# Optimization experiments

Hardware: AMD Instinct MI355X
Metric: run time of the kernel (lower is better)

## Reference

```python
import jax, jax.numpy as jnp
import numpy as np

B, N_GENES, N_SETS, G = 256, 10000, 1000, 128   # batch, input_dim, output_dim, geneset_size
H1, H2 = 64, 32                                  # hidden_dims
EPS = 1e-5                                       # BatchNorm1d eps


def _batchnorm(h, gamma, beta):
    # BatchNorm1d in training mode: biased batch stats over the batch axis
    mean = jnp.mean(h, axis=0, keepdims=True)
    var = jnp.mean(jnp.square(h - mean), axis=0, keepdims=True)
    return (h - mean) * jax.lax.rsqrt(var + EPS) * gamma + beta


def setup_inputs() -> dict:
    key = jax.random.key(0)
    ks = jax.random.split(key, 7)
    # Adjacency with exactly G distinct ones per column -> gather index list [N_SETS, G]
    rng = np.random.default_rng(0)
    gene_idx = np.argsort(rng.random((N_SETS, N_GENES)), axis=1)[:, :G]
    gene_idx = jnp.asarray(np.sort(gene_idx, axis=1), dtype=jnp.int32)

    x = jax.random.normal(ks[0], (B, N_GENES), jnp.float32)
    s1, s2, s3 = 1.0 / np.sqrt(G), 1.0 / np.sqrt(H1), 1.0 / np.sqrt(H2)
    W1 = jax.random.uniform(ks[1], (N_SETS, G, H1), jnp.float32, -s1, s1)
    b1 = jax.random.uniform(ks[2], (N_SETS, H1), jnp.float32, -s1, s1)
    W2 = jax.random.uniform(ks[3], (N_SETS, H1, H2), jnp.float32, -s2, s2)
    b2 = jax.random.uniform(ks[4], (N_SETS, H2), jnp.float32, -s2, s2)
    W3 = jax.random.uniform(ks[5], (N_SETS, H2), jnp.float32, -s3, s3)
    b3 = jax.random.uniform(ks[6], (N_SETS,), jnp.float32, -s3, s3)
    g1 = jnp.ones((N_SETS, H1), jnp.float32)
    be1 = jnp.zeros((N_SETS, H1), jnp.float32)
    g2 = jnp.ones((N_SETS, H2), jnp.float32)
    be2 = jnp.zeros((N_SETS, H2), jnp.float32)
    return {"x": x, "gene_idx": gene_idx, "W1": W1, "b1": b1, "g1": g1, "be1": be1,
            "W2": W2, "b2": b2, "g2": g2, "be2": be2, "W3": W3, "b3": b3}


def reference(x, gene_idx, W1, b1, g1, be1, W2, b2, g2, be2, W3, b3):
    # Per-geneset gather: x[:, adj[:,i]==1] for all i at once -> [B, S, G]
    xg = x[:, gene_idx]
    # Linear -> ReLU -> BatchNorm (per geneset, grouped GEMM)
    h = jax.nn.relu(jnp.einsum('bsg,sgh->bsh', xg, W1) + b1)
    h = _batchnorm(h, g1, be1)
    h = jax.nn.relu(jnp.einsum('bsh,shk->bsk', h, W2) + b2)
    h = _batchnorm(h, g2, be2)
    # Final Linear(H2 -> 1) -> ReLU, concatenated over genesets -> [B, S]
    out = jax.nn.relu(jnp.einsum('bsh,sh->bs', h, W3) + b3)
    return out
```

## Files before the change

kernel.cpp:

```cpp
#include <hip/hip_runtime.h>
#include <stdint.h>

#define BB 256
#define NG 10000
#define NS 1000
#define GG 128
#define H1 64
#define H2 32
#define EPSV 1e-5f


typedef unsigned short ushortT;
typedef __attribute__((ext_vector_type(4))) short short4v;
typedef __attribute__((ext_vector_type(8))) short short8v;
typedef __attribute__((ext_vector_type(4))) float float4v;

__device__ __forceinline__ float bf2f(ushortT u) {
    union { uint32_t i; float f; } v; v.i = ((uint32_t)u) << 16; return v.f;
}
__device__ __forceinline__ ushortT f2bf(float f) {
    union { float f; uint32_t i; } v; v.f = f;
    uint32_t x = v.i;
    return (ushortT)((x + 0x7fffu + ((x >> 16) & 1u)) >> 16);
}
__device__ __forceinline__ uint32_t pack2(ushortT lo, ushortT hi) {
    return (uint32_t)lo | ((uint32_t)hi << 16);
}
__device__ __forceinline__ bool probe_f32(const void* g1) {
    return ((*(const uint32_t*)g1) & 0xFFFFu) == 0u;
}
__device__ __forceinline__ float loadf(const void* p, int i, bool isf) {
    return isf ? ((const float*)p)[i] : bf2f(((const ushortT*)p)[i]);
}
__device__ __forceinline__ ushortT loadbf(const void* p, size_t i, bool isf) {
    return isf ? f2bf(((const float*)p)[i]) : ((const ushortT*)p)[i];
}

__global__ __launch_bounds__(256) void k_transpose(const void* __restrict__ x,
                                                   ushortT* __restrict__ xT,
                                                   const void* __restrict__ g1p) {
    __shared__ ushortT tile[64][66];
    const bool isf = probe_f32(g1p);
    const int tx = threadIdx.x & 63;
    const int tz = threadIdx.x >> 6;
    const int j0 = blockIdx.x * 64;
    const int b0 = blockIdx.y * 64;
    const int j = j0 + tx;
#pragma unroll
    for (int k = 0; k < 16; ++k) {
        int bl = tz * 16 + k;
        ushortT v = 0;
        if (j < NG) v = loadbf(x, (size_t)(b0 + bl) * NG + j, isf);
        tile[bl][tx] = v;
    }
    __syncthreads();
#pragma unroll
    for (int k = 0; k < 16; ++k) {
        int jl = tz * 16 + k;
        int jw = j0 + jl;
        if (jw < NG) xT[jw * BB + b0 + tx] = tile[tx][jl];
    }
}

__global__ __launch_bounds__(256, 4) void k_main(
    const ushortT* __restrict__ xT, const int* __restrict__ gidx,
    const void* __restrict__ W1, const void* __restrict__ W2,
    const void* __restrict__ b1, const void* __restrict__ g1, const void* __restrict__ be1,
    const void* __restrict__ b2, const void* __restrict__ g2, const void* __restrict__ be2,
    const void* __restrict__ W3, const void* __restrict__ b3,
    void* __restrict__ out) {
    __shared__ ushortT xg[BB * 68];
    __shared__ ushortT w1s[64 * 36];

    char* xgc = (char*)xg;
    float* redf = (float*)w1s;
    ushortT* w2s = w1s;

    const bool isf = probe_f32(g1);
    const int s = blockIdx.x;
    const int t = threadIdx.x;
    const int w = t >> 6;
    const int lane = t & 63;
    const int l16 = lane & 15;
    const int quad = lane >> 4;
    const size_t base1 = (size_t)s * (GG * H1);
    const size_t base2 = (size_t)s * (H1 * H2);

#define HOLEI(i)   (*(int*)(xgc + ((i) >> 1) * 136 + 128 + ((i) & 1) * 4))
#define HOLEF(r0, k) (*(float*)(xgc + ((r0) + ((k) >> 1)) * 136 + 128 + ((k) & 1) * 4))

    float b1v[4], w3v[2], b2v[2];
#pragma unroll
    for (int nt = 0; nt < 4; ++nt) b1v[nt] = loadf(b1, s * H1 + nt * 16 + l16, isf);
#pragma unroll
    for (int nt = 0; nt < 2; ++nt) {
        b2v[nt] = loadf(b2, s * H2 + nt * 16 + l16, isf);
        w3v[nt] = loadf(W3, s * H2 + nt * 16 + l16, isf);
    }
    const float b3v = loadf(b3, s, isf);
    float g1v = 0.f, be1v = 0.f, g2v = 0.f, be2v = 0.f;
    if (t < 64) { g1v = loadf(g1, s * H1 + t, isf); be1v = loadf(be1, s * H1 + t, isf); }
    if (t < 32) { g2v = loadf(g2, s * H2 + t, isf); be2v = loadf(be2, s * H2 + t, isf); }

    ushortT w2r[8];
    {
        const int k2 = t & 31, h0 = (t >> 5) * 8;
#pragma unroll
        for (int j = 0; j < 8; ++j) w2r[j] = loadbf(W2, base2 + (size_t)(h0 + j) * H2 + k2, isf);
    }

    if (t < GG) HOLEI(t) = gidx[s * GG + t];

    auto stageW1 = [&](int q) {
#pragma unroll
        for (int rep = 0; rep < 2; ++rep) {
            const int el = rep * 256 + t;
            const int e4 = q * 512 + el;
            const int g = el >> 4;
            const int h0 = (el & 15) * 4;
            ushortT u0, u1, u2, u3;
            if (isf) {
                float4 v = *(const float4*)((const float*)W1 + base1 + (size_t)e4 * 4);
                u0 = f2bf(v.x); u1 = f2bf(v.y); u2 = f2bf(v.z); u3 = f2bf(v.w);
            } else {
                uint2 v = *(const uint2*)((const ushortT*)W1 + base1 + (size_t)e4 * 4);
                u0 = (ushortT)v.x; u1 = (ushortT)(v.x >> 16);
                u2 = (ushortT)v.y; u3 = (ushortT)(v.y >> 16);
            }
            w1s[(h0 + 0) * 36 + g] = u0;
            w1s[(h0 + 1) * 36 + g] = u1;
            w1s[(h0 + 2) * 36 + g] = u2;
            w1s[(h0 + 3) * 36 + g] = u3;
        }
    };
    stageW1(0);
    __syncthreads();

    float4v acc1[4][4];
#pragma unroll
    for (int mt = 0; mt < 4; ++mt)
#pragma unroll
        for (int nt = 0; nt < 4; ++nt) acc1[mt][nt] = (float4v){0.f, 0.f, 0.f, 0.f};

#pragma unroll
    for (int c = 0; c < 2; ++c) {
#pragma unroll
        for (int gq = 0; gq < 8; ++gq) {
            const int i0 = c * 64 + gq * 8;
            int2 p0 = *(const int2*)(xgc + (i0 >> 1) * 136 + 128);
            int2 p1 = *(const int2*)(xgc + ((i0 >> 1) + 1) * 136 + 128);
            int2 p2 = *(const int2*)(xgc + ((i0 >> 1) + 2) * 136 + 128);
            int2 p3 = *(const int2*)(xgc + ((i0 >> 1) + 3) * 136 + 128);
            ushortT v0 = xT[p0.x * BB + t], v1 = xT[p0.y * BB + t];
            ushortT v2 = xT[p1.x * BB + t], v3 = xT[p1.y * BB + t];
            ushortT v4 = xT[p2.x * BB + t], v5 = xT[p2.y * BB + t];
            ushortT v6 = xT[p3.x * BB + t], v7 = xT[p3.y * BB + t];
            uint2 pa = {pack2(v0, v1), pack2(v2, v3)};
            uint2 pb = {pack2(v4, v5), pack2(v6, v7)};
            *(uint2*)(&xg[t * 68 + gq * 8]) = pa;
            *(uint2*)(&xg[t * 68 + gq * 8 + 4]) = pb;
        }
#pragma unroll
        for (int kt = 0; kt < 2; ++kt) {
            const int q = 2 * c + kt;
            if (q > 0) {
                __syncthreads();
                stageW1(q);
                __syncthreads();
            }
            short8v bfrag[4];
#pragma unroll
            for (int nt = 0; nt < 4; ++nt) {
                const int h = nt * 16 + l16;
                const int woff = h * 36 + quad * 8;
                short4v blo = *(const short4v*)(&w1s[woff]);
                short4v bhi = *(const short4v*)(&w1s[woff + 4]);
                bfrag[nt] = __builtin_shufflevector(blo, bhi, 0, 1, 2, 3, 4, 5, 6, 7);
            }
#pragma unroll
            for (int mt = 0; mt < 4; ++mt) {
                const int b = w * 64 + mt * 16 + l16;
                const ushortT* p = &xg[b * 68 + kt * 32 + quad * 8];
                short4v alo = *(const short4v*)(p);
                short4v ahi = *(const short4v*)(p + 4);
                short8v af = __builtin_shufflevector(alo, ahi, 0, 1, 2, 3, 4, 5, 6, 7);
#pragma unroll
                for (int nt = 0; nt < 4; ++nt)
                    acc1[mt][nt] = __builtin_amdgcn_mfma_f32_16x16x32_bf16(af, bfrag[nt], acc1[mt][nt], 0, 0, 0);
            }
        }
    }

    float s1v[4], s2v[4];
#pragma unroll
    for (int nt = 0; nt < 4; ++nt) {
        float s1 = 0.f, s2 = 0.f;
        const float bb = b1v[nt];
#pragma unroll
        for (int mt = 0; mt < 4; ++mt)
#pragma unroll
            for (int r = 0; r < 4; ++r) {
                float v = acc1[mt][nt][r] + bb;
                v = v > 0.f ? v : 0.f;
                s1 += v;
                s2 += v * v;
            }
        s1 += __shfl_xor(s1, 16); s1 += __shfl_xor(s1, 32);
        s2 += __shfl_xor(s2, 16); s2 += __shfl_xor(s2, 32);
        s1v[nt] = s1; s2v[nt] = s2;
    }
    __syncthreads();
    if (lane < 16) {
#pragma unroll
        for (int nt = 0; nt < 4; ++nt) {
            const int k = w * 64 + nt * 16 + lane;
            redf[k] = s1v[nt];
            redf[256 + k] = s2v[nt];
        }
    }
    __syncthreads();

    if (t < 64) {
        float ts = redf[t] + redf[64 + t] + redf[128 + t] + redf[192 + t];
        float tq = redf[256 + t] + redf[320 + t] + redf[384 + t] + redf[448 + t];
        float mean = ts * (1.0f / 256.0f);
        float var = tq * (1.0f / 256.0f) - mean * mean;
        var = var > 0.f ? var : 0.f;
        float rs = rsqrtf(var + EPSV);
        float a = g1v * rs;
        HOLEF(64, t) = a;
        HOLEF(96, t) = be1v - mean * a;
    }
    __syncthreads();

    {
        const int k2 = t & 31, h0 = (t >> 5) * 8;
        uint4 pk;
        pk.x = pack2(w2r[0], w2r[1]);
        pk.y = pack2(w2r[2], w2r[3]);
        pk.z = pack2(w2r[4], w2r[5]);
        pk.w = pack2(w2r[6], w2r[7]);
        *(uint4*)(&w2s[k2 * 72 + h0]) = pk;
    }
#pragma unroll
    for (int nt = 0; nt < 4; ++nt) {
        const int h = nt * 16 + l16;
        const float bb = b1v[nt];
        const float a = HOLEF(64, h), cc = HOLEF(96, h);
#pragma unroll
        for (int mt = 0; mt < 4; ++mt)
#pragma unroll
            for (int r = 0; r < 4; ++r) {
                const int b = w * 64 + mt * 16 + quad * 4 + r;
                float v = acc1[mt][nt][r] + bb;
                v = v > 0.f ? v : 0.f;
                xg[b * 68 + h] = f2bf(v * a + cc);
            }
    }
    __syncthreads();

    float4v acc2[4][2];
#pragma unroll
    for (int mt = 0; mt < 4; ++mt)
#pragma unroll
        for (int nt = 0; nt < 2; ++nt) acc2[mt][nt] = (float4v){0.f, 0.f, 0.f, 0.f};

#pragma unroll
    for (int kt = 0; kt < 2; ++kt) {
        const int kl = kt * 32 + quad * 8;
        short8v bfrag2[2];
#pragma unroll
        for (int nt = 0; nt < 2; ++nt) {
            const int k2 = nt * 16 + l16;
            const int woff = k2 * 72 + kl;
            short4v blo = *(const short4v*)(&w2s[woff]);
            short4v bhi = *(const short4v*)(&w2s[woff + 4]);
            bfrag2[nt] = __builtin_shufflevector(blo, bhi, 0, 1, 2, 3, 4, 5, 6, 7);
        }
#pragma unroll
        for (int mt = 0; mt < 4; ++mt) {
            const int b = w * 64 + mt * 16 + l16;
            const ushortT* p = &xg[b * 68 + kl];
            short4v alo = *(const short4v*)(p);
            short4v ahi = *(const short4v*)(p + 4);
            short8v af = __builtin_shufflevector(alo, ahi, 0, 1, 2, 3, 4, 5, 6, 7);
#pragma unroll
            for (int nt = 0; nt < 2; ++nt)
                acc2[mt][nt] = __builtin_amdgcn_mfma_f32_16x16x32_bf16(af, bfrag2[nt], acc2[mt][nt], 0, 0, 0);
        }
    }

#pragma unroll
    for (int nt = 0; nt < 2; ++nt) {
        float s1 = 0.f, s2 = 0.f;
        const float bb = b2v[nt];
#pragma unroll
        for (int mt = 0; mt < 4; ++mt)
#pragma unroll
            for (int r = 0; r < 4; ++r) {
                float v = acc2[mt][nt][r] + bb;
                v = v > 0.f ? v : 0.f;
                s1 += v;
                s2 += v * v;
            }
        s1 += __shfl_xor(s1, 16); s1 += __shfl_xor(s1, 32);
        s2 += __shfl_xor(s2, 16); s2 += __shfl_xor(s2, 32);
        if (lane < 16) {
            const int k = w * 32 + nt * 16 + lane;
            HOLEF(0, k) = s1;
            HOLEF(64, k) = s2;
        }
    }
    __syncthreads();

    if (t < 32) {
        float ts = HOLEF(0, t) + HOLEF(0, 32 + t) + HOLEF(0, 64 + t) + HOLEF(0, 96 + t);
        float tq = HOLEF(64, t) + HOLEF(64, 32 + t) + HOLEF(64, 64 + t) + HOLEF(64, 96 + t);
        float mean = ts * (1.0f / 256.0f);
        float var = tq * (1.0f / 256.0f) - mean * mean;
        var = var > 0.f ? var : 0.f;
        float rs = rsqrtf(var + EPSV);
        float a = g2v * rs;
        HOLEF(128, t) = a;
        HOLEF(144, t) = be2v - mean * a;
    }
    __syncthreads();

    float a2[2], c2[2];
#pragma unroll
    for (int nt = 0; nt < 2; ++nt) {
        const int k2 = nt * 16 + l16;
        a2[nt] = HOLEF(128, k2);
        c2[nt] = HOLEF(144, k2);
    }
#pragma unroll
    for (int mt = 0; mt < 4; ++mt)
#pragma unroll
        for (int r = 0; r < 4; ++r) {
            float tot = 0.f;
#pragma unroll
            for (int nt = 0; nt < 2; ++nt) {
                float v = acc2[mt][nt][r] + b2v[nt];
                v = v > 0.f ? v : 0.f;
                tot += (v * a2[nt] + c2[nt]) * w3v[nt];
            }
            tot += __shfl_xor(tot, 1);
            tot += __shfl_xor(tot, 2);
            tot += __shfl_xor(tot, 4);
            tot += __shfl_xor(tot, 8);
            if (l16 == 0) {
                const int b = w * 64 + mt * 16 + quad * 4 + r;
                float o = tot + b3v;
                o = o > 0.f ? o : 0.f;
                if (isf) ((float*)out)[b * NS + s] = o;
                else     ((ushortT*)out)[b * NS + s] = f2bf(o);
            }
        }
#undef HOLEI
#undef HOLEF
}

extern "C" void kernel_launch(void* const* d_in, const int* in_sizes, int n_in,
                              void* d_out, int out_size, void* d_ws, size_t ws_size,
                              hipStream_t stream) {
    const int* gi = (const int*)d_in[1];
    ushortT* xT = (ushortT*)d_ws;

    dim3 gT((NG + 63) / 64, BB / 64);
    k_transpose<<<gT, 256, 0, stream>>>(d_in[0], xT, d_in[4]);
    k_main<<<NS, 256, 0, stream>>>(xT, gi, d_in[2], d_in[6],
                                   d_in[3], d_in[4], d_in[5],
                                   d_in[7], d_in[8], d_in[9], d_in[10], d_in[11],
                                   d_out);
}
```

Baseline: 141.9 us.

## Double-buffer W1 staging to overlap loads with MFMA and cut barriers

Result: slower. 152.3 us (+7.3%).

```diff
diff --git a/kernel.cpp b/kernel.cpp
--- a/kernel.cpp
+++ b/kernel.cpp
@@ -1,4 +1,5 @@
 #include <hip/hip_runtime.h>
+#include <hip/hip_bf16.h>
 #include <stdint.h>
 
 #define BB 256
@@ -19,9 +20,9 @@
     union { uint32_t i; float f; } v; v.i = ((uint32_t)u) << 16; return v.f;
 }
 __device__ __forceinline__ ushortT f2bf(float f) {
-    union { float f; uint32_t i; } v; v.f = f;
-    uint32_t x = v.i;
-    return (ushortT)((x + 0x7fffu + ((x >> 16) & 1u)) >> 16);
+    union { __hip_bfloat16 h; ushortT u; } cv;
+    cv.h = __float2bfloat16(f);
+    return cv.u;
 }
 __device__ __forceinline__ uint32_t pack2(ushortT lo, ushortT hi) {
     return (uint32_t)lo | ((uint32_t)hi << 16);
@@ -62,7 +63,7 @@
     }
 }
 
-__global__ __launch_bounds__(256, 4) void k_main(
+__global__ __launch_bounds__(256, 3) void k_main(
     const ushortT* __restrict__ xT, const int* __restrict__ gidx,
     const void* __restrict__ W1, const void* __restrict__ W2,
     const void* __restrict__ b1, const void* __restrict__ g1, const void* __restrict__ be1,
@@ -70,11 +71,11 @@
     const void* __restrict__ W3, const void* __restrict__ b3,
     void* __restrict__ out) {
     __shared__ ushortT xg[BB * 68];
-    __shared__ ushortT w1s[64 * 36];
+    __shared__ ushortT w1s[2][64 * 36];
 
     char* xgc = (char*)xg;
     float* redf = (float*)w1s;
-    ushortT* w2s = w1s;
+    ushortT* w2s = (ushortT*)w1s;
 
     const bool isf = probe_f32(g1);
     const int s = blockIdx.x;
@@ -86,7 +87,7 @@
     const size_t base1 = (size_t)s * (GG * H1);
     const size_t base2 = (size_t)s * (H1 * H2);
 
-#define HOLEI(i)   (*(int*)(xgc + ((i) >> 1) * 136 + 128 + ((i) & 1) * 4))
+#define HOLEI(i)     (*(int*)(xgc + ((i) >> 1) * 136 + 128 + ((i) & 1) * 4))
 #define HOLEF(r0, k) (*(float*)(xgc + ((r0) + ((k) >> 1)) * 136 + 128 + ((k) & 1) * 4))
 
     float b1v[4], w3v[2], b2v[2];
@@ -111,7 +112,7 @@
 
     if (t < GG) HOLEI(t) = gidx[s * GG + t];
 
-    auto stageW1 = [&](int q) {
+    auto stageW1 = [&](int q, ushortT* dst) {
 #pragma unroll
         for (int rep = 0; rep < 2; ++rep) {
             const int el = rep * 256 + t;
@@ -127,13 +128,13 @@
                 u0 = (ushortT)v.x; u1 = (ushortT)(v.x >> 16);
                 u2 = (ushortT)v.y; u3 = (ushortT)(v.y >> 16);
             }
-            w1s[(h0 + 0) * 36 + g] = u0;
-            w1s[(h0 + 1) * 36 + g] = u1;
-            w1s[(h0 + 2) * 36 + g] = u2;
-            w1s[(h0 + 3) * 36 + g] = u3;
+            dst[(h0 + 0) * 36 + g] = u0;
+            dst[(h0 + 1) * 36 + g] = u1;
+            dst[(h0 + 2) * 36 + g] = u2;
+            dst[(h0 + 3) * 36 + g] = u3;
         }
     };
-    stageW1(0);
+    stageW1(0, w1s[0]);
     __syncthreads();
 
     float4v acc1[4][4];
@@ -143,52 +144,51 @@
         for (int nt = 0; nt < 4; ++nt) acc1[mt][nt] = (float4v){0.f, 0.f, 0.f, 0.f};
 
 #pragma unroll
-    for (int c = 0; c < 2; ++c) {
-#pragma unroll
-        for (int gq = 0; gq < 8; ++gq) {
-            const int i0 = c * 64 + gq * 8;
-            int2 p0 = *(const int2*)(xgc + (i0 >> 1) * 136 + 128);
-            int2 p1 = *(const int2*)(xgc + ((i0 >> 1) + 1) * 136 + 128);
-            int2 p2 = *(const int2*)(xgc + ((i0 >> 1) + 2) * 136 + 128);
-            int2 p3 = *(const int2*)(xgc + ((i0 >> 1) + 3) * 136 + 128);
-            ushortT v0 = xT[p0.x * BB + t], v1 = xT[p0.y * BB + t];
-            ushortT v2 = xT[p1.x * BB + t], v3 = xT[p1.y * BB + t];
-            ushortT v4 = xT[p2.x * BB + t], v5 = xT[p2.y * BB + t];
-            ushortT v6 = xT[p3.x * BB + t], v7 = xT[p3.y * BB + t];
-            uint2 pa = {pack2(v0, v1), pack2(v2, v3)};
-            uint2 pb = {pack2(v4, v5), pack2(v6, v7)};
-            *(uint2*)(&xg[t * 68 + gq * 8]) = pa;
-            *(uint2*)(&xg[t * 68 + gq * 8 + 4]) = pb;
-        }
-#pragma unroll
-        for (int kt = 0; kt < 2; ++kt) {
-            const int q = 2 * c + kt;
-            if (q > 0) {
-                __syncthreads();
-                stageW1(q);
-                __syncthreads();
-            }
-            short8v bfrag[4];
-#pragma unroll
-            for (int nt = 0; nt < 4; ++nt) {
-                const int h = nt * 16 + l16;
-                const int woff = h * 36 + quad * 8;
-                short4v blo = *(const short4v*)(&w1s[woff]);
-                short4v bhi = *(const short4v*)(&w1s[woff + 4]);
-                bfrag[nt] = __builtin_shufflevector(blo, bhi, 0, 1, 2, 3, 4, 5, 6, 7);
-            }
-#pragma unroll
-            for (int mt = 0; mt < 4; ++mt) {
-                const int b = w * 64 + mt * 16 + l16;
-                const ushortT* p = &xg[b * 68 + kt * 32 + quad * 8];
-                short4v alo = *(const short4v*)(p);
-                short4v ahi = *(const short4v*)(p + 4);
-                short8v af = __builtin_shufflevector(alo, ahi, 0, 1, 2, 3, 4, 5, 6, 7);
-#pragma unroll
-                for (int nt = 0; nt < 4; ++nt)
-                    acc1[mt][nt] = __builtin_amdgcn_mfma_f32_16x16x32_bf16(af, bfrag[nt], acc1[mt][nt], 0, 0, 0);
-            }
-        }
+    for (int q = 0; q < 4; ++q) {
+        if ((q & 1) == 0) {
+            const int c = q >> 1;
+#pragma unroll
+            for (int gq = 0; gq < 8; ++gq) {
+                const int i0 = c * 64 + gq * 8;
+                int2 p0 = *(const int2*)(xgc + (i0 >> 1) * 136 + 128);
+                int2 p1 = *(const int2*)(xgc + ((i0 >> 1) + 1) * 136 + 128);
+                int2 p2 = *(const int2*)(xgc + ((i0 >> 1) + 2) * 136 + 128);
+                int2 p3 = *(const int2*)(xgc + ((i0 >> 1) + 3) * 136 + 128);
+                ushortT v0 = xT[p0.x * BB + t], v1 = xT[p0.y * BB + t];
+                ushortT v2 = xT[p1.x * BB + t], v3 = xT[p1.y * BB + t];
+                ushortT v4 = xT[p2.x * BB + t], v5 = xT[p2.y * BB + t];
+                ushortT v6 = xT[p3.x * BB + t], v7 = xT[p3.y * BB + t];
+                uint2 pa = {pack2(v0, v1), pack2(v2, v3)};
+                uint2 pb = {pack2(v4, v5), pack2(v6, v7)};
+                *(uint2*)(&xg[t * 68 + gq * 8]) = pa;
+                *(uint2*)(&xg[t * 68 + gq * 8 + 4]) = pb;
+            }
+        }
+        if (q < 3) stageW1(q + 1, w1s[(q + 1) & 1]);
+
+        const ushortT* wbuf = w1s[q & 1];
+        const int kt = q & 1;
+        short8v bfrag[4];
+#pragma unroll
+        for (int nt = 0; nt < 4; ++nt) {
+            const int h = nt * 16 + l16;
+            const int woff = h * 36 + quad * 8;
+            short4v blo = *(const short4v*)(&wbuf[woff]);
+            short4v bhi = *(const short4v*)(&wbuf[woff + 4]);
+            bfrag[nt] = __builtin_shufflevector(blo, bhi, 0, 1, 2, 3, 4, 5, 6, 7);
+        }
+#pragma unroll
+        for (int mt = 0; mt < 4; ++mt) {
+            const int b = w * 64 + mt * 16 + l16;
+            const ushortT* p = &xg[b * 68 + kt * 32 + quad * 8];
+            short4v alo = *(const short4v*)(p);
+            short4v ahi = *(const short4v*)(p + 4);
+            short8v af = __builtin_shufflevector(alo, ahi, 0, 1, 2, 3, 4, 5, 6, 7);
+#pragma unroll
+            for (int nt = 0; nt < 4; ++nt)
+                acc1[mt][nt] = __builtin_amdgcn_mfma_f32_16x16x32_bf16(af, bfrag[nt], acc1[mt][nt], 0, 0, 0);
+        }
+        if (q < 3) __syncthreads();
     }
 
     float s1v[4], s2v[4];
```
